# Optimization experiments

Measured on AMD Instinct MI355X. Metric: run time of the kernel, lower is better.

Reference implementation:

```python
import jax, jax.numpy as jnp
import numpy as np

EPS = 1e-6
B, T, D = 8, 4096, 512


def setup_inputs() -> dict:
    key = jax.random.key(0)
    ks = jax.random.split(key, 8)
    s = 1.0 / np.sqrt(D)
    return {
        "summarization": jax.random.normal(ks[0], (B, D), jnp.float32),
        "decoder_output": jax.random.normal(ks[1], (B, T, D), jnp.float32),
        "W_hist": jax.random.normal(ks[2], (D, D), jnp.float32) * s,
        "b_hist": jnp.zeros((D,), jnp.float32),
        "W1": jax.random.normal(ks[3], (D, D), jnp.float32) * s,
        "W2": jax.random.normal(ks[4], (D, D), jnp.float32) * s,
        "W_out": jax.random.normal(ks[5], (D, D), jnp.float32) * s,
        "b_out": jnp.zeros((D,), jnp.float32),
        "gamma": jnp.ones((D,), jnp.float32),
        "beta": jnp.zeros((D,), jnp.float32),
    }


def reference(summarization, decoder_output, W_hist, b_hist, W1, W2, W_out, b_out, gamma, beta):
    # Causal running mean: equivalent to tril-mask bmm / row-count, but O(T).
    tgt_len = decoder_output.shape[1]
    counts = jnp.arange(1, tgt_len + 1, dtype=decoder_output.dtype)[None, :, None]
    history = jnp.cumsum(decoder_output, axis=1) / counts            # [B,T,D]
    history = jnp.tanh(history @ W_hist + b_hist)                    # history_linear + tanh
    # TransformMinus: linear1(summ) - linear2(history), then linear_out + tanh
    summ_proj = (summarization @ W1)[:, None, :]                     # [B,1,D] broadcasts over T
    out = summ_proj - history @ W2
    future = jnp.tanh(out @ W_out + b_out)
    # LayerPostprocessing (eval: dropout = identity): LayerNorm(future + decoder_output)
    x = future + decoder_output
    mu = jnp.mean(x, axis=-1, keepdims=True)
    var = jnp.mean(jnp.square(x - mu), axis=-1, keepdims=True)
    return (x - mu) / jnp.sqrt(var + EPS) * gamma + beta
```

## Files before the change

### kernel.cpp

```cpp
#include <hip/hip_runtime.h>
#include <hip/hip_bf16.h>
#include <stdint.h>
#include <stddef.h>

#define DEV static __device__ __forceinline__

typedef __attribute__((ext_vector_type(8))) short short8;
typedef __attribute__((ext_vector_type(4))) float floatx4;

constexpr int Tn = 4096, Dn = 512;
constexpr int NC = 128, CTm = 32;

union U8s { uint4 u4; unsigned short us[8]; };
union U4f { float4 f4; float f[4]; };
union U4s { uint2 u2; unsigned short us[4]; };

DEV float b2f(unsigned short u) {
  union { unsigned int i; float f; } c; c.i = ((unsigned int)u) << 16; return c.f;
}
DEV unsigned short f2b(float f) {
  union { float f; unsigned int u; } c; c.f = f;
  unsigned int r = c.u + 0x7fffu + ((c.u >> 16) & 1u);
  return (unsigned short)(r >> 16);
}
DEV float fast_tanh(float x) {
  float e = __expf(2.0f * x);
  return 1.0f - 2.0f / (e + 1.0f);
}

typedef __attribute__((address_space(1))) void GVOID;
typedef __attribute__((address_space(3))) void LVOID;
DEV void async16(const unsigned short* g, unsigned short* l) {
  __builtin_amdgcn_global_load_lds((GVOID*)g, (LVOID*)l, 16, 0, 0);
}

__global__ void k_fuse1(const float* __restrict__ dec, float* __restrict__ part,
                        const float* __restrict__ Wh, const float* __restrict__ Wo,
                        const float* __restrict__ W1, const float* __restrict__ W2,
                        unsigned short* __restrict__ WhT, unsigned short* __restrict__ WoT,
                        unsigned short* __restrict__ W1b, unsigned short* __restrict__ W2b) {
  int blk = blockIdx.x;
  if (blk < 512) {
    int idx = blk * 256 + threadIdx.x;
    int d4 = idx & 127;
    int c  = (idx >> 7) & (NC - 1);
    int b  = idx >> 14;
    const float* p = dec + ((size_t)b * Tn + (size_t)c * CTm) * Dn + d4 * 4;
    float s[4] = {0,0,0,0};
#pragma unroll 4
    for (int i = 0; i < CTm; ++i) {
      U4f v; v.f4 = *(const float4*)(p + (size_t)i * Dn);
#pragma unroll
      for (int j = 0; j < 4; ++j) s[j] += v.f[j];
    }
    float* o = part + ((size_t)(b * NC + c)) * Dn + d4 * 4;
#pragma unroll
    for (int j = 0; j < 4; ++j) o[j] = s[j];
  } else {
    int wb = blk - 512;
    if (wb < 128) {
      const float* in = (wb < 64) ? Wh : Wo;
      unsigned short* out = (wb < 64) ? WhT : WoT;
      int lb = wb & 63;
      __shared__ float t[64][65];
      int n0 = (lb & 7) * 64, k0 = (lb >> 3) * 64;
#pragma unroll
      for (int l = 0; l < 16; ++l) {
        int lin = l * 256 + threadIdx.x;
        int r = lin >> 6, c = lin & 63;
        t[r][c] = in[(size_t)(k0 + r) * 512 + n0 + c];
      }
      __syncthreads();
#pragma unroll
      for (int l = 0; l < 16; ++l) {
        int lin = l * 256 + threadIdx.x;
        int r = lin >> 6, c = lin & 63;
        out[(size_t)(n0 + r) * 512 + k0 + c] = f2b(t[c][r]);
      }
    } else {
      const float* in = (wb < 160) ? W1 : W2;
      unsigned short* out = (wb < 160) ? W1b : W2b;
      int lb = (wb - 128) & 31;
      size_t base = ((size_t)lb * 256 + threadIdx.x) * 32;
#pragma unroll
      for (int l = 0; l < 8; ++l) {
        U4f v; v.f4 = *(const float4*)(in + base + l * 4);
        U4s o;
#pragma unroll
        for (int j = 0; j < 4; ++j) o.us[j] = f2b(v.f[j]);
        *(uint2*)(out + base + l * 4) = o.u2;
      }
    }
  }
}

template<int EPI>
DEV void gemm_core(const unsigned short* __restrict__ A,
                   const unsigned short* __restrict__ BT,
                   unsigned short* __restrict__ C,
                   const float* __restrict__ bias,
                   const float* __restrict__ spo,
                   const float* __restrict__ dec,
                   const float* __restrict__ gamma,
                   const float* __restrict__ beta,
                   float* __restrict__ out,
                   int m0) {
  __shared__ alignas(16) unsigned short sA[2][128 * 32];
  __shared__ alignas(16) unsigned short sB[2][512 * 32];
  __shared__ float lnS[128][4];
  __shared__ float lnQ[128][4];
  const int tid  = threadIdx.x;
  const int lane = tid & 63;
  const int w    = tid >> 6;
  const int wr   = w >> 2;
  const int wc   = w & 3;
  const int rs   = lane & 15;
  const int quad = lane >> 4;

  floatx4 acc[4][8];
#pragma unroll
  for (int i = 0; i < 4; ++i)
#pragma unroll
    for (int j = 0; j < 8; ++j) acc[i][j] = (floatx4){0.f, 0.f, 0.f, 0.f};

  auto STAGE = [&](int kt, int buf) {
    {
      int r = tid >> 2, c = tid & 3;
      int kc = (c ^ ((r >> 1) & 3)) * 8;
      async16(A + (size_t)(m0 + r) * 512 + kt + kc, &sA[buf][tid * 8]);
    }
#pragma unroll
    for (int l = 0; l < 4; ++l) {
      int ch = l * 512 + tid;
      int r = ch >> 2, c = ch & 3;
      int kc = (c ^ ((r >> 1) & 3)) * 8;
      async16(BT + (size_t)r * 512 + kt + kc, &sB[buf][ch * 8]);
    }
  };

  auto COMPUTE = [&](int buf) {
    __builtin_amdgcn_s_setprio(1);
    const int co = (quad ^ ((rs >> 1) & 3)) * 8;
    short8 bfr[8];
#pragma unroll
    for (int nj = 0; nj < 8; ++nj)
      bfr[nj] = *(const short8*)(&sB[buf][(wc * 128 + nj * 16 + rs) * 32 + co]);
#pragma unroll
    for (int mi = 0; mi < 4; ++mi) {
      short8 af = *(const short8*)(&sA[buf][(wr * 64 + mi * 16 + rs) * 32 + co]);
#pragma unroll
      for (int nj = 0; nj < 8; ++nj)
        acc[mi][nj] = __builtin_amdgcn_mfma_f32_16x16x32_bf16(af, bfr[nj], acc[mi][nj], 0, 0, 0);
    }
    __builtin_amdgcn_s_setprio(0);
  };

  STAGE(0, 0);
  for (int t = 0; t < 15; ++t) {
    STAGE((t + 1) * 32, (t + 1) & 1);
    asm volatile("s_waitcnt vmcnt(5)\n\ts_barrier" ::: "memory");
    COMPUTE(t & 1);
    asm volatile("s_barrier" ::: "memory");
  }
  asm volatile("s_waitcnt vmcnt(0)\n\ts_barrier" ::: "memory");
  COMPUTE(1);

  if constexpr (EPI == 0 || EPI == 2) {
#pragma unroll
    for (int nj = 0; nj < 8; ++nj) {
      const int colg = wc * 128 + nj * 16 + rs;
      float bb = (EPI == 0) ? bias[colg] : 0.f;
#pragma unroll
      for (int mi = 0; mi < 4; ++mi) {
#pragma unroll
        for (int r = 0; r < 4; ++r) {
          const int rowg = m0 + wr * 64 + mi * 16 + quad * 4 + r;
          float v = acc[mi][nj][r];
          if constexpr (EPI == 0) v = fast_tanh(v + bb);
          C[(size_t)rowg * 512 + colg] = f2b(v);
        }
      }
    }
  } else {
    const int bidx = m0 >> 12;
    float spv[8], gv[8], bv[8];
    int colv[8];
#pragma unroll
    for (int nj = 0; nj < 8; ++nj) {
      colv[nj] = wc * 128 + nj * 16 + rs;
      spv[nj] = spo[bidx * Dn + colv[nj]];
      gv[nj]  = gamma[colv[nj]];
      bv[nj]  = beta[colv[nj]];
    }
#pragma unroll
    for (int mi = 0; mi < 4; ++mi) {
#pragma unroll
      for (int r = 0; r < 4; ++r) {
        const int lrow = wr * 64 + mi * 16 + quad * 4 + r;
        const size_t rowg = (size_t)(m0 + lrow);
        float s = 0.f, sq = 0.f;
#pragma unroll
        for (int nj = 0; nj < 8; ++nj) {
          float dv = dec[rowg * 512 + colv[nj]];
          float xf = fast_tanh(spv[nj] - acc[mi][nj][r]) + dv;
          acc[mi][nj][r] = xf;
          s += xf; sq += xf * xf;
        }
#pragma unroll
        for (int o = 8; o > 0; o >>= 1) { s += __shfl_xor(s, o, 64); sq += __shfl_xor(sq, o, 64); }
        if (rs == 0) { lnS[lrow][wc] = s; lnQ[lrow][wc] = sq; }
      }
    }
    __syncthreads();
#pragma unroll
    for (int mi = 0; mi < 4; ++mi) {
#pragma unroll
      for (int r = 0; r < 4; ++r) {
        const int lrow = wr * 64 + mi * 16 + quad * 4 + r;
        const size_t rowg = (size_t)(m0 + lrow);
        float s = 0.f, sq = 0.f;
#pragma unroll
        for (int k = 0; k < 4; ++k) { s += lnS[lrow][k]; sq += lnQ[lrow][k]; }
        float mu   = s * (1.0f / 512.0f);
        float var  = sq * (1.0f / 512.0f) - mu * mu;
        float rstd = rsqrtf(var + 1e-6f);
#pragma unroll
        for (int nj = 0; nj < 8; ++nj)
          out[rowg * 512 + colv[nj]] = (acc[mi][nj][r] - mu) * rstd * gv[nj] + bv[nj];
      }
    }
  }
}

__global__ __launch_bounds__(512, 1)
void k_gemmH(const unsigned short* __restrict__ A, const unsigned short* __restrict__ BT,
             unsigned short* __restrict__ C, const float* __restrict__ bias) {
  gemm_core<0>(A, BT, C, bias, nullptr, nullptr, nullptr, nullptr, nullptr,
               blockIdx.x * 128);
}

__global__ __launch_bounds__(512, 1)
void k_gemmFLN(const unsigned short* __restrict__ A, const unsigned short* __restrict__ BT,
               const float* __restrict__ spo, const float* __restrict__ dec,
               const float* __restrict__ gamma, const float* __restrict__ beta,
               float* __restrict__ out) {
  gemm_core<5>(A, BT, nullptr, nullptr, spo, dec, gamma, beta, out,
               blockIdx.x * 128);
}

__global__ __launch_bounds__(512, 1)
void k_wgemm2(const unsigned short* __restrict__ WoT,
              const unsigned short* __restrict__ W2b, const unsigned short* __restrict__ W1b,
              unsigned short* __restrict__ W2WoT, unsigned short* __restrict__ W1WoT,
              float* __restrict__ part) {
  int blk = blockIdx.x;
  if (blk < 8) {
    const unsigned short* BT = (blk & 4) ? W1b : W2b;
    unsigned short* Cc = (blk & 4) ? W1WoT : W2WoT;
    gemm_core<2>(WoT, BT, Cc, nullptr, nullptr, nullptr, nullptr, nullptr, nullptr,
                 (blk & 3) * 128);
  } else {
    int idx = (blk - 8) * 512 + threadIdx.x;
    int d4 = idx & 127;
    int b  = idx >> 7;
    float* p = part + (size_t)b * NC * Dn + d4 * 4;
    float s[4] = {0, 0, 0, 0};
    for (int c0 = 0; c0 < NC; c0 += 8) {
      U4f v[8];
#pragma unroll
      for (int i = 0; i < 8; ++i) v[i].f4 = *(const float4*)(p + (size_t)(c0 + i) * Dn);
#pragma unroll
      for (int i = 0; i < 8; ++i) {
        U4f o;
#pragma unroll
        for (int j = 0; j < 4; ++j) { o.f[j] = s[j]; s[j] += v[i].f[j]; }
        *(float4*)(p + (size_t)(c0 + i) * Dn) = o.f4;
      }
    }
  }
}

__global__ void k_fuse3(const float* __restrict__ dec, const float* __restrict__ part,
                        unsigned short* __restrict__ M,
                        const float* __restrict__ summ,
                        const unsigned short* __restrict__ W1WoT,
                        const float* __restrict__ bo, float* __restrict__ spo) {
  int blk = blockIdx.x;
  if (blk < 512) {
    int idx = blk * 256 + threadIdx.x;
    int d4 = idx & 127;
    int c  = (idx >> 7) & (NC - 1);
    int b  = idx >> 14;
    size_t rbase = (size_t)b * Tn + (size_t)c * CTm;
    U4f s; s.f4 = *(const float4*)(part + ((size_t)b * NC + c) * Dn + d4 * 4);
    int t0 = c * CTm;
    const float* dp = dec + rbase * Dn + d4 * 4;
    unsigned short* mp = M + rbase * Dn + d4 * 4;
#pragma unroll 4
    for (int i = 0; i < CTm; ++i) {
      U4f v; v.f4 = *(const float4*)(dp + (size_t)i * Dn);
      float inv = 1.0f / (float)(t0 + i + 1);
      U4s o;
#pragma unroll
      for (int j = 0; j < 4; ++j) { s.f[j] += v.f[j]; o.us[j] = f2b(s.f[j] * inv); }
      *(uint2*)(mp + (size_t)i * Dn) = o.u2;
    }
  } else {
    int widx = (blk - 512) * 4 + (threadIdx.x >> 6);
    int lane = threadIdx.x & 63;
    int n = widx & 511; int b = widx >> 9;
    U8s w8; w8.u4 = *(const uint4*)(W1WoT + (size_t)n * Dn + lane * 8);
    U4f s0, s1;
    s0.f4 = *(const float4*)(summ + (size_t)b * Dn + lane * 8);
    s1.f4 = *(const float4*)(summ + (size_t)b * Dn + lane * 8 + 4);
    float acc = 0.f;
#pragma unroll
    for (int j = 0; j < 4; ++j) acc += s0.f[j] * b2f(w8.us[j]);
#pragma unroll
    for (int j = 0; j < 4; ++j) acc += s1.f[j] * b2f(w8.us[j + 4]);
#pragma unroll
    for (int o = 32; o > 0; o >>= 1) acc += __shfl_xor(acc, o, 64);
    if (lane == 0) spo[(size_t)b * Dn + n] = acc + bo[n];
  }
}

extern "C" void kernel_launch(void* const* d_in, const int* in_sizes, int n_in,
                              void* d_out, int out_size, void* d_ws, size_t ws_size,
                              hipStream_t stream) {
  (void)in_sizes; (void)n_in; (void)out_size; (void)ws_size;
  const float* summ = (const float*)d_in[0];
  const float* dec  = (const float*)d_in[1];
  const float* Wh   = (const float*)d_in[2];
  const float* bh   = (const float*)d_in[3];
  const float* W1   = (const float*)d_in[4];
  const float* W2   = (const float*)d_in[5];
  const float* Wo   = (const float*)d_in[6];
  const float* bo   = (const float*)d_in[7];
  const float* gam  = (const float*)d_in[8];
  const float* bet  = (const float*)d_in[9];
  float* out = (float*)d_out;

  char* ws = (char*)d_ws;
  unsigned short* Mbuf  = (unsigned short*)(ws);
  unsigned short* Hbuf  = (unsigned short*)(ws + 33554432);
  float*          part  = (float*)(ws + 67108864);
  float*          spo   = (float*)(ws + 69206016);
  unsigned short* WhT   = (unsigned short*)(ws + 69238784);
  unsigned short* WoT   = (unsigned short*)(ws + 69763072);
  unsigned short* W2b   = (unsigned short*)(ws + 70287360);
  unsigned short* W2WoT = (unsigned short*)(ws + 70811648);
  unsigned short* W1b   = (unsigned short*)(ws + 71335936);
  unsigned short* W1WoT = (unsigned short*)(ws + 71860224);

  k_fuse1<<<704, 256, 0, stream>>>(dec, part, Wh, Wo, W1, W2, WhT, WoT, W1b, W2b);

  k_wgemm2<<<10, 512, 0, stream>>>(WoT, W2b, W1b, W2WoT, W1WoT, part);

  k_fuse3<<<1536, 256, 0, stream>>>(dec, part, Mbuf, summ, W1WoT, bo, spo);

  k_gemmH<<<256, 512, 0, stream>>>(Mbuf, WhT, Hbuf, bh);

  k_gemmFLN<<<256, 512, 0, stream>>>(Hbuf, W2WoT, spo, dec, gam, bet, out);
}
```

Before: 247.8 us.

## Split GEMMs into smaller tiles for more blocks and higher occupancy

The history GEMM becomes a standalone 128x128-tile kernel with a 2D grid of 1024 blocks of 256 threads and K-step 64. The LayerNorm GEMM and the weight-product GEMM now use 64-row tiles over the full 512 columns, which doubles the block count and raises the occupancy hint. The change gives more parallelism across the GPU's compute units and less register pressure. In exchange it drops the double-buffered async pipeline in favour of single-buffered load-wait-compute loops. It also loses the swizzle in the new H kernel, so LDS bank conflicts may rise, and the gamma, beta and spo loads are no longer hoisted.

```diff
diff --git a/kernel.cpp b/kernel.cpp
--- a/kernel.cpp
+++ b/kernel.cpp
@@ -94,21 +94,84 @@
   }
 }
 
+__global__ __launch_bounds__(256, 2)
+void k_gemmH(const unsigned short* __restrict__ A, const unsigned short* __restrict__ BT,
+             unsigned short* __restrict__ C, const float* __restrict__ bias) {
+  __shared__ alignas(16) unsigned short sA[128 * 64];
+  __shared__ alignas(16) unsigned short sB[128 * 64];
+  const int m0 = blockIdx.x * 128, n0 = blockIdx.y * 128;
+  const int tid  = threadIdx.x;
+  const int lane = tid & 63;
+  const int w    = tid >> 6;
+  const int wm   = (w >> 1) * 64;
+  const int wn   = (w & 1) * 64;
+  const int rs   = lane & 15;
+  const int quad = lane >> 4;
+
+  floatx4 acc[4][4];
+#pragma unroll
+  for (int i = 0; i < 4; ++i)
+#pragma unroll
+    for (int j = 0; j < 4; ++j) acc[i][j] = (floatx4){0.f, 0.f, 0.f, 0.f};
+
+  for (int kt = 0; kt < 512; kt += 64) {
+#pragma unroll
+    for (int l = 0; l < 4; ++l) {
+      int ch = l * 256 + tid;
+      int r = ch >> 3, kc = ch & 7;
+      async16(A  + (size_t)(m0 + r) * 512 + kt + kc * 8, sA + (size_t)ch * 8);
+      async16(BT + (size_t)(n0 + r) * 512 + kt + kc * 8, sB + (size_t)ch * 8);
+    }
+    asm volatile("s_waitcnt vmcnt(0)" ::: "memory");
+    __syncthreads();
+
+#pragma unroll
+    for (int kk = 0; kk < 2; ++kk) {
+      const int kb = kk * 32 + quad * 8;
+      short8 af[4], bfr[4];
+#pragma unroll
+      for (int i = 0; i < 4; ++i)
+        af[i] = *(const short8*)(sA + (size_t)(wm + i * 16 + rs) * 64 + kb);
+#pragma unroll
+      for (int j = 0; j < 4; ++j)
+        bfr[j] = *(const short8*)(sB + (size_t)(wn + j * 16 + rs) * 64 + kb);
+#pragma unroll
+      for (int i = 0; i < 4; ++i)
+#pragma unroll
+        for (int j = 0; j < 4; ++j)
+          acc[i][j] = __builtin_amdgcn_mfma_f32_16x16x32_bf16(af[i], bfr[j], acc[i][j], 0, 0, 0);
+    }
+    __syncthreads();
+  }
+
+#pragma unroll
+  for (int i = 0; i < 4; ++i) {
+#pragma unroll
+    for (int j = 0; j < 4; ++j) {
+      const int colg = n0 + wn + j * 16 + rs;
+#pragma unroll
+      for (int r = 0; r < 4; ++r) {
+        const int rowg = m0 + wm + i * 16 + quad * 4 + r;
+        C[(size_t)rowg * 512 + colg] = f2b(fast_tanh(acc[i][j][r] + bias[colg]));
+      }
+    }
+  }
+}
+
 template<int EPI>
-DEV void gemm_core(const unsigned short* __restrict__ A,
-                   const unsigned short* __restrict__ BT,
-                   unsigned short* __restrict__ C,
-                   const float* __restrict__ bias,
-                   const float* __restrict__ spo,
-                   const float* __restrict__ dec,
-                   const float* __restrict__ gamma,
-                   const float* __restrict__ beta,
-                   float* __restrict__ out,
-                   int m0) {
-  __shared__ alignas(16) unsigned short sA[2][128 * 32];
-  __shared__ alignas(16) unsigned short sB[2][512 * 32];
-  __shared__ float lnS[128][4];
-  __shared__ float lnQ[128][4];
+DEV void gemm64_core(const unsigned short* __restrict__ A,
+                     const unsigned short* __restrict__ BT,
+                     unsigned short* __restrict__ C,
+                     const float* __restrict__ spo,
+                     const float* __restrict__ dec,
+                     const float* __restrict__ gamma,
+                     const float* __restrict__ beta,
+                     float* __restrict__ out,
+                     int m0) {
+  __shared__ alignas(16) unsigned short sA[64 * 32];
+  __shared__ alignas(16) unsigned short sB[512 * 32];
+  __shared__ float lnS[64][4];
+  __shared__ float lnQ[64][4];
   const int tid  = threadIdx.x;
   const int lane = tid & 63;
   const int w    = tid >> 6;
@@ -117,92 +180,69 @@
   const int rs   = lane & 15;
   const int quad = lane >> 4;
 
-  floatx4 acc[4][8];
-#pragma unroll
-  for (int i = 0; i < 4; ++i)
+  floatx4 acc[2][8];
+#pragma unroll
+  for (int i = 0; i < 2; ++i)
 #pragma unroll
     for (int j = 0; j < 8; ++j) acc[i][j] = (floatx4){0.f, 0.f, 0.f, 0.f};
 
-  auto STAGE = [&](int kt, int buf) {
-    {
+  for (int t = 0; t < 16; ++t) {
+    const int kt = t * 32;
+    if (tid < 256) {
       int r = tid >> 2, c = tid & 3;
       int kc = (c ^ ((r >> 1) & 3)) * 8;
-      async16(A + (size_t)(m0 + r) * 512 + kt + kc, &sA[buf][tid * 8]);
+      async16(A + (size_t)(m0 + r) * 512 + kt + kc, &sA[tid * 8]);
     }
 #pragma unroll
     for (int l = 0; l < 4; ++l) {
       int ch = l * 512 + tid;
       int r = ch >> 2, c = ch & 3;
       int kc = (c ^ ((r >> 1) & 3)) * 8;
-      async16(BT + (size_t)r * 512 + kt + kc, &sB[buf][ch * 8]);
-    }
-  };
-
-  auto COMPUTE = [&](int buf) {
-    __builtin_amdgcn_s_setprio(1);
+      async16(BT + (size_t)r * 512 + kt + kc, &sB[ch * 8]);
+    }
+    asm volatile("s_waitcnt vmcnt(0)" ::: "memory");
+    __syncthreads();
+
     const int co = (quad ^ ((rs >> 1) & 3)) * 8;
-    short8 bfr[8];
-#pragma unroll
-    for (int nj = 0; nj < 8; ++nj)
-      bfr[nj] = *(const short8*)(&sB[buf][(wc * 128 + nj * 16 + rs) * 32 + co]);
-#pragma unroll
-    for (int mi = 0; mi < 4; ++mi) {
-      short8 af = *(const short8*)(&sA[buf][(wr * 64 + mi * 16 + rs) * 32 + co]);
-#pragma unroll
-      for (int nj = 0; nj < 8; ++nj)
-        acc[mi][nj] = __builtin_amdgcn_mfma_f32_16x16x32_bf16(af, bfr[nj], acc[mi][nj], 0, 0, 0);
-    }
-    __builtin_amdgcn_s_setprio(0);
-  };
-
-  STAGE(0, 0);
-  for (int t = 0; t < 15; ++t) {
-    STAGE((t + 1) * 32, (t + 1) & 1);
-    asm volatile("s_waitcnt vmcnt(5)\n\ts_barrier" ::: "memory");
-    COMPUTE(t & 1);
-    asm volatile("s_barrier" ::: "memory");
-  }
-  asm volatile("s_waitcnt vmcnt(0)\n\ts_barrier" ::: "memory");
-  COMPUTE(1);
-
-  if constexpr (EPI == 0 || EPI == 2) {
+    short8 af0 = *(const short8*)(&sA[(wr * 32 + rs) * 32 + co]);
+    short8 af1 = *(const short8*)(&sA[(wr * 32 + 16 + rs) * 32 + co]);
+#pragma unroll
+    for (int nj = 0; nj < 8; ++nj) {
+      short8 bf = *(const short8*)(&sB[(wc * 128 + nj * 16 + rs) * 32 + co]);
+      acc[0][nj] = __builtin_amdgcn_mfma_f32_16x16x32_bf16(af0, bf, acc[0][nj], 0, 0, 0);
+      acc[1][nj] = __builtin_amdgcn_mfma_f32_16x16x32_bf16(af1, bf, acc[1][nj], 0, 0, 0);
+    }
+    __syncthreads();
+  }
+
+  if constexpr (EPI == 2) {
 #pragma unroll
     for (int nj = 0; nj < 8; ++nj) {
       const int colg = wc * 128 + nj * 16 + rs;
-      float bb = (EPI == 0) ? bias[colg] : 0.f;
-#pragma unroll
-      for (int mi = 0; mi < 4; ++mi) {
+#pragma unroll
+      for (int mi = 0; mi < 2; ++mi) {
 #pragma unroll
         for (int r = 0; r < 4; ++r) {
-          const int rowg = m0 + wr * 64 + mi * 16 + quad * 4 + r;
-          float v = acc[mi][nj][r];
-          if constexpr (EPI == 0) v = fast_tanh(v + bb);
-          C[(size_t)rowg * 512 + colg] = f2b(v);
+          const int rowg = m0 + wr * 32 + mi * 16 + quad * 4 + r;
+          C[(size_t)rowg * 512 + colg] = f2b(acc[mi][nj][r]);
         }
       }
     }
   } else {
     const int bidx = m0 >> 12;
-    float spv[8], gv[8], bv[8];
-    int colv[8];
-#pragma unroll
-    for (int nj = 0; nj < 8; ++nj) {
-      colv[nj] = wc * 128 + nj * 16 + rs;
-      spv[nj] = spo[bidx * Dn + colv[nj]];
-      gv[nj]  = gamma[colv[nj]];
-      bv[nj]  = beta[colv[nj]];
-    }
-#pragma unroll
-    for (int mi = 0; mi < 4; ++mi) {
+#pragma unroll
+    for (int mi = 0; mi < 2; ++mi) {
 #pragma unroll
       for (int r = 0; r < 4; ++r) {
-        const int lrow = wr * 64 + mi * 16 + quad * 4 + r;
+        const int lrow = wr * 32 + mi * 16 + quad * 4 + r;
         const size_t rowg = (size_t)(m0 + lrow);
         float s = 0.f, sq = 0.f;
 #pragma unroll
         for (int nj = 0; nj < 8; ++nj) {
-          float dv = dec[rowg * 512 + colv[nj]];
-          float xf = fast_tanh(spv[nj] - acc[mi][nj][r]) + dv;
+          const int colg = wc * 128 + nj * 16 + rs;
+          float sp = spo[bidx * Dn + colg];
+          float dv = dec[rowg * 512 + colg];
+          float xf = fast_tanh(sp - acc[mi][nj][r]) + dv;
           acc[mi][nj][r] = xf;
           s += xf; sq += xf * xf;
         }
@@ -213,10 +253,10 @@
     }
     __syncthreads();
 #pragma unroll
-    for (int mi = 0; mi < 4; ++mi) {
+    for (int mi = 0; mi < 2; ++mi) {
 #pragma unroll
       for (int r = 0; r < 4; ++r) {
-        const int lrow = wr * 64 + mi * 16 + quad * 4 + r;
+        const int lrow = wr * 32 + mi * 16 + quad * 4 + r;
         const size_t rowg = (size_t)(m0 + lrow);
         float s = 0.f, sq = 0.f;
 #pragma unroll
@@ -225,42 +265,36 @@
         float var  = sq * (1.0f / 512.0f) - mu * mu;
         float rstd = rsqrtf(var + 1e-6f);
 #pragma unroll
-        for (int nj = 0; nj < 8; ++nj)
-          out[rowg * 512 + colv[nj]] = (acc[mi][nj][r] - mu) * rstd * gv[nj] + bv[nj];
-      }
-    }
-  }
-}
-
-__global__ __launch_bounds__(512, 1)
-void k_gemmH(const unsigned short* __restrict__ A, const unsigned short* __restrict__ BT,
-             unsigned short* __restrict__ C, const float* __restrict__ bias) {
-  gemm_core<0>(A, BT, C, bias, nullptr, nullptr, nullptr, nullptr, nullptr,
-               blockIdx.x * 128);
-}
-
-__global__ __launch_bounds__(512, 1)
+        for (int nj = 0; nj < 8; ++nj) {
+          const int colg = wc * 128 + nj * 16 + rs;
+          out[rowg * 512 + colg] = (acc[mi][nj][r] - mu) * rstd * gamma[colg] + beta[colg];
+        }
+      }
+    }
+  }
+}
+
+__global__ __launch_bounds__(512, 4)
 void k_gemmFLN(const unsigned short* __restrict__ A, const unsigned short* __restrict__ BT,
                const float* __restrict__ spo, const float* __restrict__ dec,
                const float* __restrict__ gamma, const float* __restrict__ beta,
                float* __restrict__ out) {
-  gemm_core<5>(A, BT, nullptr, nullptr, spo, dec, gamma, beta, out,
-               blockIdx.x * 128);
-}
-
-__global__ __launch_bounds__(512, 1)
+  gemm64_core<5>(A, BT, nullptr, spo, dec, gamma, beta, out, blockIdx.x * 64);
+}
+
+__global__ __launch_bounds__(512, 4)
 void k_wgemm2(const unsigned short* __restrict__ WoT,
               const unsigned short* __restrict__ W2b, const unsigned short* __restrict__ W1b,
               unsigned short* __restrict__ W2WoT, unsigned short* __restrict__ W1WoT,
               float* __restrict__ part) {
   int blk = blockIdx.x;
-  if (blk < 8) {
-    const unsigned short* BT = (blk & 4) ? W1b : W2b;
-    unsigned short* Cc = (blk & 4) ? W1WoT : W2WoT;
-    gemm_core<2>(WoT, BT, Cc, nullptr, nullptr, nullptr, nullptr, nullptr, nullptr,
-                 (blk & 3) * 128);
+  if (blk < 16) {
+    const unsigned short* BT = (blk & 8) ? W1b : W2b;
+    unsigned short* Cc = (blk & 8) ? W1WoT : W2WoT;
+    gemm64_core<2>(WoT, BT, Cc, nullptr, nullptr, nullptr, nullptr, nullptr,
+                   (blk & 7) * 64);
   } else {
-    int idx = (blk - 8) * 512 + threadIdx.x;
+    int idx = (blk - 16) * 512 + threadIdx.x;
     int d4 = idx & 127;
     int b  = idx >> 7;
     float* p = part + (size_t)b * NC * Dn + d4 * 4;
@@ -354,11 +388,11 @@
 
   k_fuse1<<<704, 256, 0, stream>>>(dec, part, Wh, Wo, W1, W2, WhT, WoT, W1b, W2b);
 
-  k_wgemm2<<<10, 512, 0, stream>>>(WoT, W2b, W1b, W2WoT, W1WoT, part);
+  k_wgemm2<<<18, 512, 0, stream>>>(WoT, W2b, W1b, W2WoT, W1WoT, part);
 
   k_fuse3<<<1536, 256, 0, stream>>>(dec, part, Mbuf, summ, W1WoT, bo, spo);
 
-  k_gemmH<<<256, 512, 0, stream>>>(Mbuf, WhT, Hbuf, bh);
-
-  k_gemmFLN<<<256, 512, 0, stream>>>(Hbuf, W2WoT, spo, dec, gam, bet, out);
-}
+  k_gemmH<<<dim3(256, 4), 256, 0, stream>>>(Mbuf, WhT, Hbuf, bh);
+
+  k_gemmFLN<<<512, 512, 0, stream>>>(Hbuf, W2WoT, spo, dec, gam, bet, out);
+}
```

Measured after the change: 234.8 us. 1.06x faster.
